# Kernel optimization log

Hardware: AMD Instinct MI355X
Metric: run time of the kernel (lower is better)

Reference implementation:

```python
import jax, jax.numpy as jnp
import numpy as np

EPS = 1e-6

def _ln2d(x, w, b):
    # LayerNorm2d: normalize over channel dim per pixel
    mu = x.mean(axis=1, keepdims=True)
    var = ((x - mu) ** 2).mean(axis=1, keepdims=True)
    return (x - mu) / jnp.sqrt(var + EPS) * w[None, :, None, None] + b[None, :, None, None]

def _conv1x1(x, w, b):
    return jnp.einsum('oc,bchw->bohw', w, x) + b[None, :, None, None]

def setup_inputs() -> dict:
    key = jax.random.key(0)
    ks = jax.random.split(key, 20)
    B, c, H, W = 4, 32, 256, 256
    dw = 2 * c
    k, wH, wW = 3, 32, 32
    s = 0.05
    d = {}
    d['inp'] = jax.random.normal(ks[0], (B, c, H, W), jnp.float32)
    d['conv2_weight'] = jax.random.normal(ks[1], (B, dw, k, k, wH, wW), jnp.float32) * 0.1
    d['conv1_w'] = jax.random.normal(ks[2], (dw, c), jnp.float32) * s
    d['conv1_b'] = jnp.zeros((dw,), jnp.float32)
    d['conv3_w'] = jax.random.normal(ks[3], (c, c), jnp.float32) * s
    d['conv3_b'] = jnp.zeros((c,), jnp.float32)
    d['sca_w'] = jax.random.normal(ks[4], (c, c), jnp.float32) * s
    d['sca_b'] = jnp.zeros((c,), jnp.float32)
    d['conv4_w'] = jax.random.normal(ks[5], (dw, c), jnp.float32) * s
    d['conv4_b'] = jnp.zeros((dw,), jnp.float32)
    d['conv5_w'] = jax.random.normal(ks[6], (c, c), jnp.float32) * s
    d['conv5_b'] = jnp.zeros((c,), jnp.float32)
    d['norm1_w'] = jnp.ones((c,), jnp.float32)
    d['norm1_b'] = jnp.zeros((c,), jnp.float32)
    d['norm2_w'] = jnp.ones((c,), jnp.float32)
    d['norm2_b'] = jnp.zeros((c,), jnp.float32)
    # original inits these to zero; use small random so the block is non-trivial
    d['beta'] = jax.random.normal(ks[7], (1, c, 1, 1), jnp.float32) * 0.1
    d['gamma'] = jax.random.normal(ks[8], (1, c, 1, 1), jnp.float32) * 0.1
    return d

def reference(inp, conv2_weight, conv1_w, conv1_b, conv3_w, conv3_b, sca_w, sca_b,
              conv4_w, conv4_b, conv5_w, conv5_b, norm1_w, norm1_b, norm2_w, norm2_b,
              beta, gamma):
    B, c, H, W = inp.shape
    x = _ln2d(inp, norm1_w, norm1_b)
    x = _conv1x1(x, conv1_w, conv1_b)                 # [B, 2c, H, W]
    Bw, C, kH, kW, wH, wW = conv2_weight.shape
    # bilinear upsample (half-pixel centers, == torch align_corners=False)
    w2 = conv2_weight.reshape(B * C, kH * kW, wH, wW)
    w2 = jax.image.resize(w2, (B * C, kH * kW, H, W), method='linear')
    w2 = w2.reshape(B, C, kH * kW, H, W)
    # ddf with all-ones channel filter + 'mul' == per-pixel spatial 3x3 conv per channel
    pad = kH // 2
    xp = jnp.pad(x, ((0, 0), (0, 0), (pad, pad), (pad, pad)))
    patches = jnp.stack([xp[:, :, i:i + H, j:j + W]
                         for i in range(kH) for j in range(kW)], axis=2)  # [B,2c,9,H,W]
    x = (patches * w2).sum(axis=2)                    # [B, 2c, H, W]
    x1, x2 = jnp.split(x, 2, axis=1)                  # SimpleGate
    x = x1 * x2                                       # [B, c, H, W]
    s = _conv1x1(x.mean(axis=(2, 3), keepdims=True), sca_w, sca_b)
    x = x * s
    x = _conv1x1(x, conv3_w, conv3_b)
    y = inp + x * beta
    x = _conv1x1(_ln2d(y, norm2_w, norm2_b), conv4_w, conv4_b)
    x1, x2 = jnp.split(x, 2, axis=1)
    x = _conv1x1(x1 * x2, conv5_w, conv5_b)
    return y + x * gamma
```

## Files before the change

kernel.cpp:

```cpp
#include <hip/hip_runtime.h>
#include <hip/hip_bf16.h>

typedef __hip_bfloat16 bf16;
typedef __attribute__((ext_vector_type(8))) unsigned short u16x8;
typedef __attribute__((ext_vector_type(8))) short s16x8;
typedef __attribute__((ext_vector_type(4))) float f32x4;
typedef __attribute__((ext_vector_type(4))) unsigned short us16x4;

#define B_   4
#define C_   32
#define DW_  64
#define H_   256
#define W_   256
#define P_   65536
#define SRC_ 32
#define TRS_ 272
#define TPL_ 70176

#define OW1    0
#define OB1    2048
#define OW3    2112
#define OB3    3136
#define OWS    3168
#define OBS    4192
#define OW4    4224
#define OB4    6272
#define OW5    6336
#define OB5    7360
#define ON1W   7392
#define ON1B   7424
#define ON2W   7456
#define ON2B   7488
#define OBETA  7520
#define OGAMMA 7552
#define OSUMS  7584
#define OSVEC  7712
#define OFLAG  7900
#define CWF_BOFF 32768ull
#define T1_BOFF  (CWF_BOFF + 9437184ull)
#define G_BOFF   (T1_BOFF + 35930112ull)

__device__ __forceinline__ bf16  f2b(float v){ return __float2bfloat16(v); }
__device__ __forceinline__ float bfu(unsigned short u){ return __uint_as_float(((unsigned int)u) << 16); }
__device__ __forceinline__ unsigned short fbits(float v){
    bf16 b = __float2bfloat16(v);
    return *reinterpret_cast<unsigned short*>(&b);
}

template<typename T> __device__ __forceinline__ float ldf(const T* p);
template<> __device__ __forceinline__ float ldf<float>(const float* p){ return *p; }
template<> __device__ __forceinline__ float ldf<bf16>(const bf16* p){ return __bfloat162float(*p); }

template<typename T> struct dtag;
template<> struct dtag<float>{ static constexpr int v = 0; };
template<> struct dtag<bf16>{ static constexpr int v = 1; };

__device__ __forceinline__ f32x4 MF(s16x8 a, s16x8 b, f32x4 c){
    return __builtin_amdgcn_mfma_f32_16x16x32_bf16(a, b, c, 0, 0, 0);
}
__device__ __forceinline__ s16x8 wfrag8(const float* p){
    float4 a = *(const float4*)p;
    float4 c = *(const float4*)(p + 4);
    s16x8 r;
    r[0] = (short)fbits(a.x); r[1] = (short)fbits(a.y);
    r[2] = (short)fbits(a.z); r[3] = (short)fbits(a.w);
    r[4] = (short)fbits(c.x); r[5] = (short)fbits(c.y);
    r[6] = (short)fbits(c.z); r[7] = (short)fbits(c.w);
    return r;
}

__global__ void k_detect(const unsigned short* __restrict__ raw, int* __restrict__ flag)
{
    int t = threadIdx.x;
    int bad = 0;
    for (int k = 0; k < 8; ++k) {
        unsigned short u = raw[2 * (t + 64 * k)];
        float v = __uint_as_float(((unsigned int)u) << 16);
        if (!(fabsf(v) < 1e6f)) bad = 1;
    }
    int anybad = __any(bad);
    if (t == 0) *flag = anybad ? 0 : 1;
}

template<typename T>
__global__ void k_prep(const T* __restrict__ w1, const T* __restrict__ b1,
                       const T* __restrict__ w3, const T* __restrict__ b3,
                       const T* __restrict__ wsc, const T* __restrict__ bsc_,
                       const T* __restrict__ w4, const T* __restrict__ b4,
                       const T* __restrict__ w5, const T* __restrict__ b5,
                       const T* __restrict__ n1w, const T* __restrict__ n1b,
                       const T* __restrict__ n2w, const T* __restrict__ n2b,
                       const T* __restrict__ bet, const T* __restrict__ gam,
                       float* __restrict__ wsf, const int* __restrict__ flag)
{
    if (*flag != dtag<T>::v) return;
    int t = threadIdx.x;
    for (int i = t; i < 2048; i += 256) wsf[OW1 + i] = ldf<T>(w1 + i);
    for (int i = t; i < 64;   i += 256) wsf[OB1 + i] = ldf<T>(b1 + i);
    for (int i = t; i < 1024; i += 256) wsf[OW3 + i] = ldf<T>(w3 + i);
    for (int i = t; i < 32;   i += 256) wsf[OB3 + i] = ldf<T>(b3 + i);
    for (int i = t; i < 1024; i += 256) wsf[OWS + i] = ldf<T>(wsc + i);
    for (int i = t; i < 32;   i += 256) wsf[OBS + i] = ldf<T>(bsc_ + i);
    for (int i = t; i < 2048; i += 256) wsf[OW4 + i] = ldf<T>(w4 + i);
    for (int i = t; i < 64;   i += 256) wsf[OB4 + i] = ldf<T>(b4 + i);
    for (int i = t; i < 1024; i += 256) wsf[OW5 + i] = ldf<T>(w5 + i);
    for (int i = t; i < 32;   i += 256) wsf[OB5 + i] = ldf<T>(b5 + i);
    for (int i = t; i < 32;   i += 256) wsf[ON1W + i] = ldf<T>(n1w + i);
    for (int i = t; i < 32;   i += 256) wsf[ON1B + i] = ldf<T>(n1b + i);
    for (int i = t; i < 32;   i += 256) wsf[ON2W + i] = ldf<T>(n2w + i);
    for (int i = t; i < 32;   i += 256) wsf[ON2B + i] = ldf<T>(n2b + i);
    for (int i = t; i < 32;   i += 256) wsf[OBETA + i] = ldf<T>(bet + i);
    for (int i = t; i < 32;   i += 256) wsf[OGAMMA + i] = ldf<T>(gam + i);
    for (int i = t; i < 128;  i += 256) wsf[OSUMS + i] = 0.f;
}

__global__ void k_cwf(const void* __restrict__ cw, float* __restrict__ cwfT,
                      const int* __restrict__ flag)
{
    int o = blockIdx.x * 256 + threadIdx.x;
    int p   = o & 63;
    int t2  = o >> 6;
    int tap = t2 % 9;
    int t3  = t2 / 9;
    int b   = t3 >> 10;
    int rc  = t3 & 1023;
    int cg  = p >> 3;
    int chq = (p >> 2) & 1;
    int ch4 = p & 3;
    int oc  = chq * 32 + cg * 4 + ch4;
    size_t iidx = ((size_t)(b * DW_ + oc) * 9 + tap) * 1024 + rc;
    float v;
    if (*flag == 0) v = ((const float*)cw)[iidx];
    else            v = bfu(((const unsigned short*)cw)[iidx]);
    cwfT[o] = v;
}

#define OSTR1_ 280
template<typename T>
__device__ __forceinline__ void ln1_body(const T* __restrict__ inp,
        const float* __restrict__ wsf, bf16* __restrict__ t1p,
        short* __restrict__ xsh, short* __restrict__ osh)
{
    const int t = threadIdx.x;
    const int b = blockIdx.x >> 8;
    const int h = blockIdx.x & 255;
    const int p0 = h << 8;

    {
        const T* ip = inp + (size_t)(b * C_) * P_ + p0 + t;
        float v[C_];
        float m = 0.f;
        #pragma unroll
        for (int ch = 0; ch < C_; ++ch) { v[ch] = ldf<T>(ip + (size_t)ch * P_); m += v[ch]; }
        m *= (1.f / C_);
        float var = 0.f;
        #pragma unroll
        for (int ch = 0; ch < C_; ++ch) { float d = v[ch] - m; var += d * d; }
        var *= (1.f / C_);
        float inv = rsqrtf(var + 1e-6f);
        u16x8* xr = (u16x8*)(xsh + t * 32);
        #pragma unroll
        for (int qq = 0; qq < 4; ++qq) {
            u16x8 vv;
            #pragma unroll
            for (int j = 0; j < 8; ++j) {
                int ch = qq * 8 + j;
                vv[j] = fbits((v[ch] - m) * inv * wsf[ON1W + ch] + wsf[ON1B + ch]);
            }
            xr[qq] = vv;
        }
        int och = t >> 4, cc = t & 15;
        osh[och * OSTR1_ + (cc == 0 ? 0 : 256 + cc)] = 0;
    }
    __syncthreads();

    const int lane = t & 63, wv = t >> 6;
    const int l15 = lane & 15, l4 = lane >> 4;
    const int wp0 = wv * 64;

    s16x8 w1f[4];
    f32x4 b1v[4];
    #pragma unroll
    for (int m = 0; m < 4; ++m) {
        w1f[m] = wfrag8(wsf + OW1 + (m * 16 + l15) * 32 + l4 * 8);
        b1v[m] = *(const f32x4*)(wsf + OB1 + m * 16 + l4 * 4);
    }
    s16x8 xb[4];
    #pragma unroll
    for (int tn = 0; tn < 4; ++tn)
        xb[tn] = *(const s16x8*)(xsh + (wp0 + tn * 16 + l15) * 32 + l4 * 8);

    const size_t prow = (size_t)(b * DW_) * TPL_ + (size_t)(h + 1) * TRS_;
    #pragma unroll
    for (int m = 0; m < 4; ++m) {
        #pragma unroll
        for (int tn = 0; tn < 4; ++tn) {
            f32x4 acc = MF(w1f[m], xb[tn], b1v[m]);
            int px = wp0 + tn * 16 + l15;
            #pragma unroll
            for (int i = 0; i < 4; ++i)
                osh[(l4 * 4 + i) * OSTR1_ + 1 + px] = (short)fbits(acc[i]);
        }
        __syncthreads();
        for (int it = 0; it < 3; ++it) {
            int idx = it * 256 + t;
            if (idx < 544) {
                int och = idx / 34, ck = idx - och * 34;
                u16x8 v = *(const u16x8*)(osh + och * OSTR1_ + ck * 8);
                *(u16x8*)((unsigned short*)t1p + prow + (size_t)(m * 16 + och) * TPL_ + ck * 8) = v;
            }
        }
        __syncthreads();
    }

    if (h == 0 || h == 255) {
        size_t rbase = (size_t)(b * DW_) * TPL_ + (h == 0 ? 0 : (size_t)257 * TRS_);
        u16x8 z;
        #pragma unroll
        for (int j = 0; j < 8; ++j) z[j] = 0;
        for (int it = 0; it < 9; ++it) {
            int idx = it * 256 + t;
            if (idx < 2176) {
                int och = idx / 34, ck = idx - och * 34;
                *(u16x8*)((unsigned short*)t1p + rbase + (size_t)och * TPL_ + ck * 8) = z;
            }
        }
    }
}

__global__ __launch_bounds__(256, 4) void k_ln1_conv1(const void* __restrict__ inp,
        const float* __restrict__ wsf, bf16* __restrict__ t1p,
        const int* __restrict__ flag)
{
    __shared__ short xsh[256 * 32];
    __shared__ short osh[16 * OSTR1_];
    if (*flag == 0) ln1_body<float>((const float*)inp, wsf, t1p, xsh, osh);
    else            ln1_body<bf16>((const bf16*)inp, wsf, t1p, xsh, osh);
}

#define G_ 4
__global__ __launch_bounds__(256, 4) void k_ddf(const unsigned short* __restrict__ t1u,
        const float* __restrict__ cwfT, bf16* __restrict__ g, float* __restrict__ sums)
{
    __shared__ float CWs[4320];

    int bid = blockIdx.x;
    int tile = bid & 31;
    int cg  = (bid >> 5) & 7;
    int b   = bid >> 8;
    int th = tile >> 2, tw = tile & 3;
    int cellh0 = th * 4;
    int cellw0 = tw * 8;
    int cp0 = cg * G_;

    {
        const float* cb = cwfT + (size_t)b * 589824;
        for (int it = 0; it < 17; ++it) {
            int idx = it * 256 + threadIdx.x;
            if (idx < 4320) {
                int chp = idx & 7;
                int t2  = idx >> 3;
                int tap = t2 % 9;
                int t3  = t2 / 9;
                int cc  = t3 % 10;
                int rr  = t3 / 10;
                int cr = cellh0 - 1 + rr; cr = cr < 0 ? 0 : (cr > 31 ? 31 : cr);
                int cw = cellw0 - 1 + cc; cw = cw < 0 ? 0 : (cw > 31 ? 31 : cw);
                CWs[chp * 540 + tap * 60 + rr * 10 + cc] =
                    cb[(size_t)(cr * 32 + cw) * 576 + tap * 64 + cg * 8 + chp];
            }
        }
    }
    __syncthreads();

    int lane = threadIdx.x & 63, wid = threadIdx.x >> 6;
    int k = lane >> 3, r = lane & 7;
    int cellh = cellh0 + wid;
    int h = cellh * 8 + r;
    int w = (cellw0 + k) * 8;

    int rsel = r >> 2;
    float fh = rsel ? ((float)r * 0.125f - 0.4375f) : ((float)r * 0.125f + 0.5625f);
    float gh = 1.f - fh;
    int rr0k = (wid + rsel) * 10 + k;

    const unsigned short* tb = t1u + (size_t)(b * DW_) * TPL_ + (size_t)h * TRS_ + w;
    bf16* gp = g + (size_t)(b * C_) * P_ + h * 256 + w;

    for (int l = 0; l < G_; ++l) {
        int cp = cp0 + l;
        const unsigned short* pl1 = tb + (size_t)cp * TPL_;
        const unsigned short* pl2 = pl1 + (size_t)C_ * TPL_;
        const float* q1 = CWs + l * 540;
        const float* q2 = CWs + (G_ + l) * 540;

        float acc1[8], acc2[8];
        #pragma unroll
        for (int pass = 0; pass < 2; ++pass) {
            const unsigned short* pl = pass ? pl2 : pl1;
            const float* q = pass ? q2 : q1;
            float* acc = pass ? acc2 : acc1;

            u16x8 v8[3];
            unsigned int ve[3];
            #pragma unroll
            for (int i = 0; i < 3; ++i) {
                const unsigned short* rp = pl + i * TRS_;
                v8[i] = *(const u16x8*)rp;
                ve[i] = *(const unsigned int*)(rp + 8);
            }
            float S00[8], S01[8], S10[8], S11[8];
            #pragma unroll
            for (int c = 0; c < 8; ++c) { S00[c]=0.f; S01[c]=0.f; S10[c]=0.f; S11[c]=0.f; }
            #pragma unroll
            for (int i = 0; i < 3; ++i) {
                float p[10];
                #pragma unroll
                for (int j = 0; j < 8; ++j) p[j] = bfu((unsigned short)v8[i][j]);
                p[8] = bfu((unsigned short)(ve[i] & 0xFFFFu));
                p[9] = bfu((unsigned short)(ve[i] >> 16));
                #pragma unroll
                for (int j = 0; j < 3; ++j) {
                    const float* qb = q + (i * 3 + j) * 60 + rr0k;
                    float w00 = qb[0],  w01 = qb[1],  w02 = qb[2];
                    float w10 = qb[10], w11 = qb[11], w12 = qb[12];
                    #pragma unroll
                    for (int c = 0; c < 8; ++c) {
                        float pv = p[c + j];
                        S00[c] += pv * ((c < 4) ? w00 : w01);
                        S01[c] += pv * ((c < 4) ? w01 : w02);
                        S10[c] += pv * ((c < 4) ? w10 : w11);
                        S11[c] += pv * ((c < 4) ? w11 : w12);
                    }
                }
            }
            const float fwt[8] = {0.5625f, 0.6875f, 0.8125f, 0.9375f,
                                  0.0625f, 0.1875f, 0.3125f, 0.4375f};
            #pragma unroll
            for (int c = 0; c < 8; ++c) {
                float fw = fwt[c], gw = 1.f - fw;
                acc[c] = gh * (gw * S00[c] + fw * S01[c]) + fh * (gw * S10[c] + fw * S11[c]);
            }
        }

        u16x8 ov;
        float s = 0.f;
        #pragma unroll
        for (int c = 0; c < 8; ++c) {
            float gv = acc1[c] * acc2[c];
            s += gv;
            bf16 bv = f2b(gv);
            ov[c] = *reinterpret_cast<unsigned short*>(&bv);
        }
        *(u16x8*)(gp + (size_t)cp * P_) = ov;

        #pragma unroll
        for (int off = 32; off >= 1; off >>= 1) s += __shfl_xor(s, off, 64);
        if (lane == 0) atomicAdd(&sums[b * C_ + cp], s);
    }
}

#define XSTR_ 32
#define ISTR_ 33
#define OSTRT_ 260

template<typename T>
__device__ __forceinline__ void tail_body(const T* __restrict__ inp,
        const bf16* __restrict__ g, const float* __restrict__ wsf,
        T* __restrict__ out, short* __restrict__ xsh, float* __restrict__ ipsh,
        float* __restrict__ svsh)
{
    const int t = threadIdx.x;
    const int b = blockIdx.x >> 8;
    const int p0 = (blockIdx.x & 255) << 8;

    if (t < 32) {
        float acc = wsf[OBS + t];
        #pragma unroll
        for (int ch = 0; ch < C_; ++ch)
            acc += wsf[OWS + t * C_ + ch] * (wsf[OSUMS + b * C_ + ch] * (1.f / (float)P_));
        svsh[t] = acc;
    }
    __syncthreads();

    {
        const unsigned short* gp = (const unsigned short*)g + (size_t)(b * C_) * P_ + p0 + t;
        unsigned short row[32];
        #pragma unroll
        for (int ch = 0; ch < C_; ++ch)
            row[ch] = fbits(bfu(gp[(size_t)ch * P_]) * svsh[ch]);
        u16x8* xr = (u16x8*)(xsh + t * XSTR_);
        #pragma unroll
        for (int qq = 0; qq < 4; ++qq) {
            u16x8 vv;
            #pragma unroll
            for (int j = 0; j < 8; ++j) vv[j] = row[qq * 8 + j];
            xr[qq] = vv;
        }
        const T* ip = inp + (size_t)(b * C_) * P_ + p0 + t;
        float* ir = ipsh + t * ISTR_;
        #pragma unroll
        for (int ch = 0; ch < C_; ++ch)
            ir[ch] = ldf<T>(ip + (size_t)ch * P_);
    }
    __syncthreads();

    const int lane = t & 63, wv = t >> 6;
    const int l15 = lane & 15, l4 = lane >> 4;
    const int wp0 = wv * 64;

    s16x8 w3f[2], w4f[4];
    #pragma unroll
    for (int m = 0; m < 2; ++m) w3f[m] = wfrag8(wsf + OW3 + (m * 16 + l15) * 32 + l4 * 8);
    #pragma unroll
    for (int m = 0; m < 4; ++m) w4f[m] = wfrag8(wsf + OW4 + (m * 16 + l15) * 32 + l4 * 8);

    f32x4 y[2][4];
    {
        f32x4 b3v[2], btv[2];
        #pragma unroll
        for (int m = 0; m < 2; ++m) {
            b3v[m] = *(const f32x4*)(wsf + OB3   + m * 16 + l4 * 4);
            btv[m] = *(const f32x4*)(wsf + OBETA + m * 16 + l4 * 4);
        }
        #pragma unroll
        for (int tn = 0; tn < 4; ++tn) {
            int px = wp0 + tn * 16 + l15;
            s16x8 xb = *(const s16x8*)(xsh + px * XSTR_ + l4 * 8);
            const float* irr = ipsh + px * ISTR_ + l4 * 4;
            #pragma unroll
            for (int m = 0; m < 2; ++m) {
                f32x4 acc = MF(w3f[m], xb, b3v[m]);
                f32x4 yy;
                #pragma unroll
                for (int i = 0; i < 4; ++i)
                    yy[i] = irr[m * 16 + i] + acc[i] * btv[m][i];
                y[m][tn] = yy;
            }
        }
    }
    __syncthreads();

    {
        f32x4 nwv[2], nbv[2];
        #pragma unroll
        for (int m = 0; m < 2; ++m) {
            nwv[m] = *(const f32x4*)(wsf + ON2W + m * 16 + l4 * 4);
            nbv[m] = *(const f32x4*)(wsf + ON2B + m * 16 + l4 * 4);
        }
        #pragma unroll
        for (int tn = 0; tn < 4; ++tn) {
            float s = 0.f;
            #pragma unroll
            for (int m = 0; m < 2; ++m)
                #pragma unroll
                for (int i = 0; i < 4; ++i) s += y[m][tn][i];
            s += __shfl_xor(s, 16);
            s += __shfl_xor(s, 32);
            float mean = s * (1.f / 32.f);
            float q = 0.f;
            #pragma unroll
            for (int m = 0; m < 2; ++m)
                #pragma unroll
                for (int i = 0; i < 4; ++i) { float d = y[m][tn][i] - mean; q += d * d; }
            q += __shfl_xor(q, 16);
            q += __shfl_xor(q, 32);
            float inv = rsqrtf(q * (1.f / 32.f) + 1e-6f);
            int px = wp0 + tn * 16 + l15;
            #pragma unroll
            for (int m = 0; m < 2; ++m) {
                us16x4 pk;
                #pragma unroll
                for (int i = 0; i < 4; ++i)
                    pk[i] = fbits((y[m][tn][i] - mean) * inv * nwv[m][i] + nbv[m][i]);
                *(us16x4*)(xsh + px * XSTR_ + m * 16 + l4 * 4) = pk;
            }
        }
    }

    {
        f32x4 b4v[4];
        #pragma unroll
        for (int m = 0; m < 4; ++m)
            b4v[m] = *(const f32x4*)(wsf + OB4 + m * 16 + l4 * 4);
        s16x8 yb[4];
        #pragma unroll
        for (int tn = 0; tn < 4; ++tn)
            yb[tn] = *(const s16x8*)(xsh + (wp0 + tn * 16 + l15) * XSTR_ + l4 * 8);
        #pragma unroll
        for (int tn = 0; tn < 4; ++tn) {
            f32x4 a4[4];
            #pragma unroll
            for (int m = 0; m < 4; ++m) a4[m] = MF(w4f[m], yb[tn], b4v[m]);
            int px = wp0 + tn * 16 + l15;
            #pragma unroll
            for (int m = 0; m < 2; ++m) {
                us16x4 pk;
                #pragma unroll
                for (int i = 0; i < 4; ++i) pk[i] = fbits(a4[m][i] * a4[m + 2][i]);
                *(us16x4*)(xsh + px * XSTR_ + m * 16 + l4 * 4) = pk;
            }
        }
    }

    {
        s16x8 w5f[2];
        #pragma unroll
        for (int m = 0; m < 2; ++m) w5f[m] = wfrag8(wsf + OW5 + (m * 16 + l15) * 32 + l4 * 8);
        f32x4 b5v[2], gmv[2];
        #pragma unroll
        for (int m = 0; m < 2; ++m) {
            b5v[m] = *(const f32x4*)(wsf + OB5    + m * 16 + l4 * 4);
            gmv[m] = *(const f32x4*)(wsf + OGAMMA + m * 16 + l4 * 4);
        }
        s16x8 ub[4];
        #pragma unroll
        for (int tn = 0; tn < 4; ++tn)
            ub[tn] = *(const s16x8*)(xsh + (wp0 + tn * 16 + l15) * XSTR_ + l4 * 8);
        float* oshf = ipsh;
        #pragma unroll
        for (int tn = 0; tn < 4; ++tn) {
            int px = wp0 + tn * 16 + l15;
            #pragma unroll
            for (int m = 0; m < 2; ++m) {
                f32x4 acc = MF(w5f[m], ub[tn], b5v[m]);
                #pragma unroll
                for (int i = 0; i < 4; ++i)
                    oshf[(m * 16 + l4 * 4 + i) * OSTRT_ + px] = y[m][tn][i] + acc[i] * gmv[m][i];
            }
        }
    }
    __syncthreads();

    {
        const float* oshf = ipsh;
        if (dtag<T>::v == 0) {
            float* of = (float*)out;
            #pragma unroll
            for (int it = 0; it < 8; ++it) {
                int idx = it * 256 + t;
                int och = idx >> 6, ck = idx & 63;
                f32x4 v = *(const f32x4*)(oshf + och * OSTRT_ + ck * 4);
                *(f32x4*)(of + (size_t)(b * C_ + och) * P_ + p0 + ck * 4) = v;
            }
        } else {
            unsigned short* ob = (unsigned short*)out;
            #pragma unroll
            for (int it = 0; it < 4; ++it) {
                int idx = it * 256 + t;
                int och = idx >> 5, ck = idx & 31;
                f32x4 a = *(const f32x4*)(oshf + och * OSTRT_ + ck * 8);
                f32x4 c = *(const f32x4*)(oshf + och * OSTRT_ + ck * 8 + 4);
                u16x8 pk;
                pk[0] = fbits(a[0]); pk[1] = fbits(a[1]); pk[2] = fbits(a[2]); pk[3] = fbits(a[3]);
                pk[4] = fbits(c[0]); pk[5] = fbits(c[1]); pk[6] = fbits(c[2]); pk[7] = fbits(c[3]);
                *(u16x8*)(ob + (size_t)(b * C_ + och) * P_ + p0 + ck * 8) = pk;
            }
        }
    }
}

__global__ __launch_bounds__(256, 3) void k_tail(const void* __restrict__ inp,
        const bf16* __restrict__ g, const float* __restrict__ wsf,
        void* __restrict__ out, const int* __restrict__ flag)
{
    __shared__ short xsh[256 * XSTR_];
    __shared__ float ipsh[256 * ISTR_];
    __shared__ float svsh[32];
    if (*flag == 0) tail_body<float>((const float*)inp, g, wsf, (float*)out, xsh, ipsh, svsh);
    else            tail_body<bf16>((const bf16*)inp, g, wsf, (bf16*)out, xsh, ipsh, svsh);
}

extern "C" void kernel_launch(void* const* d_in, const int* in_sizes, int n_in,
                              void* d_out, int out_size, void* d_ws, size_t ws_size,
                              hipStream_t stream)
{
    float* wsf = (float*)d_ws;
    char* wsb = (char*)d_ws;
    float* cwf = (float*)(wsb + CWF_BOFF);
    bf16* t1p = (bf16*)(wsb + T1_BOFF);
    bf16* g   = (bf16*)(wsb + G_BOFF);
    int* flag = (int*)(wsf + OFLAG);

    k_detect<<<1, 64, 0, stream>>>((const unsigned short*)d_in[0], flag);

    int nblk = (B_ * P_) / 256;

    k_prep<float><<<1, 256, 0, stream>>>(
        (const float*)d_in[2], (const float*)d_in[3], (const float*)d_in[4],
        (const float*)d_in[5], (const float*)d_in[6], (const float*)d_in[7],
        (const float*)d_in[8], (const float*)d_in[9], (const float*)d_in[10],
        (const float*)d_in[11], (const float*)d_in[12], (const float*)d_in[13],
        (const float*)d_in[14], (const float*)d_in[15], (const float*)d_in[16],
        (const float*)d_in[17], wsf, flag);
    k_prep<bf16><<<1, 256, 0, stream>>>(
        (const bf16*)d_in[2], (const bf16*)d_in[3], (const bf16*)d_in[4],
        (const bf16*)d_in[5], (const bf16*)d_in[6], (const bf16*)d_in[7],
        (const bf16*)d_in[8], (const bf16*)d_in[9], (const bf16*)d_in[10],
        (const bf16*)d_in[11], (const bf16*)d_in[12], (const bf16*)d_in[13],
        (const bf16*)d_in[14], (const bf16*)d_in[15], (const bf16*)d_in[16],
        (const bf16*)d_in[17], wsf, flag);

    k_cwf<<<9216, 256, 0, stream>>>(d_in[1], cwf, flag);

    k_ln1_conv1<<<nblk, 256, 0, stream>>>(d_in[0], wsf, t1p, flag);

    k_ddf<<<1024, 256, 0, stream>>>((const unsigned short*)t1p, cwf, g, wsf + OSUMS);

    k_tail<<<nblk, 256, 0, stream>>>(d_in[0], g, wsf, d_out, flag);
}
```

Baseline: 236.4 us.

## Merge weight transpose into LN1/conv1 kernel with tiled shared-memory transpose

Replaces the standalone per-element k_cwf gather kernel with a shared-memory tiled transpose and runs it as extra blocks inside the LN1+conv1 launch, so both front-stage tasks share one grid. The transpose now reads coalesced rows of the conv2 weights and writes contiguous 64-float rows. This removes one kernel launch and the strided gather reads, and lets the two independent workloads overlap on the GPU. Shared memory is now a single union buffer sized for the larger user, which could affect occupancy.

Result: faster. 229.3 us (-3.0%).

```diff
diff --git a/kernel.cpp b/kernel.cpp
--- a/kernel.cpp
+++ b/kernel.cpp
@@ -114,36 +114,41 @@
     for (int i = t; i < 128;  i += 256) wsf[OSUMS + i] = 0.f;
 }
 
-__global__ void k_cwf(const void* __restrict__ cw, float* __restrict__ cwfT,
-                      const int* __restrict__ flag)
-{
-    int o = blockIdx.x * 256 + threadIdx.x;
-    int p   = o & 63;
-    int t2  = o >> 6;
-    int tap = t2 % 9;
-    int t3  = t2 / 9;
-    int b   = t3 >> 10;
-    int rc  = t3 & 1023;
-    int cg  = p >> 3;
-    int chq = (p >> 2) & 1;
-    int ch4 = p & 3;
-    int oc  = chq * 32 + cg * 4 + ch4;
-    size_t iidx = ((size_t)(b * DW_ + oc) * 9 + tap) * 1024 + rc;
-    float v;
-    if (*flag == 0) v = ((const float*)cw)[iidx];
-    else            v = bfu(((const unsigned short*)cw)[iidx]);
-    cwfT[o] = v;
+__device__ void cwf_body(const void* __restrict__ cw, float* __restrict__ cwfT,
+                         int fl, int blk, float (*tile)[65])
+{
+    int rct = blk & 15;
+    int tap = (blk >> 4) % 9;
+    int b   = blk / 144;
+    int rc0 = rct * 64;
+    int tl  = threadIdx.x & 63;
+    int tg  = threadIdx.x >> 6;
+    #pragma unroll
+    for (int it = 0; it < 16; ++it) {
+        int oc = it * 4 + tg;
+        size_t iidx = ((size_t)(b * DW_ + oc) * 9 + tap) * 1024 + rc0 + tl;
+        tile[oc][tl] = (fl == 0) ? ((const float*)cw)[iidx]
+                                 : bfu(((const unsigned short*)cw)[iidx]);
+    }
+    __syncthreads();
+    #pragma unroll
+    for (int it = 0; it < 16; ++it) {
+        int rcl = it * 4 + tg;
+        int p = tl;
+        int oc = ((p >> 2) & 1) * 32 + (p >> 3) * 4 + (p & 3);
+        cwfT[((size_t)(b * 1024 + rc0 + rcl) * 9 + tap) * 64 + p] = tile[oc][rcl];
+    }
 }
 
 #define OSTR1_ 280
 template<typename T>
 __device__ __forceinline__ void ln1_body(const T* __restrict__ inp,
         const float* __restrict__ wsf, bf16* __restrict__ t1p,
-        short* __restrict__ xsh, short* __restrict__ osh)
+        short* __restrict__ xsh, short* __restrict__ osh, int blk)
 {
     const int t = threadIdx.x;
-    const int b = blockIdx.x >> 8;
-    const int h = blockIdx.x & 255;
+    const int b = blk >> 8;
+    const int h = blk & 255;
     const int p0 = h << 8;
 
     {
@@ -228,14 +233,22 @@
     }
 }
 
-__global__ __launch_bounds__(256, 4) void k_ln1_conv1(const void* __restrict__ inp,
-        const float* __restrict__ wsf, bf16* __restrict__ t1p,
+__global__ __launch_bounds__(256, 4) void k_front(const void* __restrict__ inp,
+        const void* __restrict__ cw, float* __restrict__ wsf,
+        float* __restrict__ cwfT, bf16* __restrict__ t1p,
         const int* __restrict__ flag)
 {
-    __shared__ short xsh[256 * 32];
-    __shared__ short osh[16 * OSTR1_];
-    if (*flag == 0) ln1_body<float>((const float*)inp, wsf, t1p, xsh, osh);
-    else            ln1_body<bf16>((const bf16*)inp, wsf, t1p, xsh, osh);
+    __shared__ char smem[25344];
+    int bid = blockIdx.x;
+    int fl = *flag;
+    if (bid < 1024) {
+        short* xsh = (short*)smem;
+        short* osh = (short*)(smem + 16384);
+        if (fl == 0) ln1_body<float>((const float*)inp, wsf, t1p, xsh, osh, bid);
+        else         ln1_body<bf16>((const bf16*)inp, wsf, t1p, xsh, osh, bid);
+    } else {
+        cwf_body(cw, cwfT, fl, bid - 1024, (float(*)[65])smem);
+    }
 }
 
 #define G_ 4
@@ -584,8 +597,6 @@
 
     k_detect<<<1, 64, 0, stream>>>((const unsigned short*)d_in[0], flag);
 
-    int nblk = (B_ * P_) / 256;
-
     k_prep<float><<<1, 256, 0, stream>>>(
         (const float*)d_in[2], (const float*)d_in[3], (const float*)d_in[4],
         (const float*)d_in[5], (const float*)d_in[6], (const float*)d_in[7],
@@ -601,11 +612,9 @@
         (const bf16*)d_in[14], (const bf16*)d_in[15], (const bf16*)d_in[16],
         (const bf16*)d_in[17], wsf, flag);
 
-    k_cwf<<<9216, 256, 0, stream>>>(d_in[1], cwf, flag);
-
-    k_ln1_conv1<<<nblk, 256, 0, stream>>>(d_in[0], wsf, t1p, flag);
+    k_front<<<1600, 256, 0, stream>>>(d_in[0], d_in[1], wsf, cwf, t1p, flag);
 
     k_ddf<<<1024, 256, 0, stream>>>((const unsigned short*)t1p, cwf, g, wsf + OSUMS);
 
-    k_tail<<<nblk, 256, 0, stream>>>(d_in[0], g, wsf, d_out, flag);
-}
+    k_tail<<<1024, 256, 0, stream>>>(d_in[0], g, wsf, d_out, flag);
+}
```
